# Performance work log

Hardware: AMD Instinct MI355X
Metric: run time of the kernel (lower is better)

## Reference

```python
import jax, jax.numpy as jnp
import numpy as np

ROUTINGS = 3
NUM_CAPSULES = 16


def squash(s, eps=1e-8):
    # s: [..., dim_capsule]
    norm = jnp.linalg.norm(s, axis=-1, keepdims=True)
    return (norm ** 2) / (1.0 + norm ** 2) * (s / (norm + eps))


def setup_inputs() -> dict:
    key = jax.random.key(0)
    k1, k2 = jax.random.split(key)
    x = jax.random.normal(k1, (64, 1024, 64), dtype=jnp.float32)      # [B, n_in, input_dim]
    weight = jax.random.normal(k2, (16, 64, 32), dtype=jnp.float32)    # [nc, input_dim, dc]
    return {"x": x, "weight": weight}


def reference(x, weight):
    B, n_in, _ = x.shape
    nc = weight.shape[0]
    # prediction vectors u_hat: [B, nc, n_in, dc]
    u_hat = jnp.einsum('bni,cid->bcnd', x, weight)
    # routing logits, softmax taken over the output-capsule axis (dim=1 in torch)
    b = jnp.zeros((B, nc, n_in, 1), dtype=u_hat.dtype)
    v = None
    for i in range(ROUTINGS):
        c = jax.nn.softmax(b, axis=1)                 # [B, nc, n_in, 1]
        s = jnp.sum(c * u_hat, axis=2)                # [B, nc, dc]
        v = squash(s)                                 # [B, nc, dc]
        if i < ROUTINGS - 1:
            # agreement: <u_hat, v> per input capsule
            b = b + jnp.einsum('bcnd,bcd->bcn', u_hat, v)[..., None]
    return v
```

## Files before the change

### kernel.cpp

```cpp
#include <hip/hip_runtime.h>
#include <math.h>

#define B_SZ 64
#define N_IN 1024
#define IDIM 64
#define NC   16
#define DC   32
#define NQ   4
#define QR   256
#define NTHR 1024
#define XS   68
#define AS   20

#define WS_CNT 0
#define WS_CS  1024
#define WS_SP1 17408
#define WS_SP2 279552

__device__ __forceinline__ void st_agent(float* p, float v) {
    __hip_atomic_store(p, v, __ATOMIC_RELAXED, __HIP_MEMORY_SCOPE_AGENT);
}
__device__ __forceinline__ float ld_agent(const float* p) {
    return __hip_atomic_load(p, __ATOMIC_RELAXED, __HIP_MEMORY_SCOPE_AGENT);
}
__device__ __forceinline__ float rdlane_f(float v, int l) {
    return __int_as_float(__builtin_amdgcn_readlane(__float_as_int(v), l));
}

__global__ __launch_bounds__(1024) void k_reset(int* cnt) {
    __hip_atomic_store(&cnt[threadIdx.x], 0, __ATOMIC_RELAXED, __HIP_MEMORY_SCOPE_AGENT);
}

__global__ __launch_bounds__(NTHR, 1)
void k_fused(const float* __restrict__ x, const float* __restrict__ W,
             float* __restrict__ out, int* __restrict__ cnt,
             float* __restrict__ cs, float* __restrict__ sp1, float* __restrict__ sp2) {
    const int b = blockIdx.x & 63, q = blockIdx.x >> 6;
    const int tid = threadIdx.x, lane = tid & 63, wave = tid >> 6;
    const int row = tid & 255, grp = tid >> 8;
    const int rq = wave & 3;

    __shared__ float __align__(16) xT[QR * XS];
    __shared__ float __align__(16) aSmT[QR * AS];
    __shared__ float __align__(16) pSm[4 * 64 * AS];
    __shared__ float __align__(16) wSm[IDIM * AS];
    __shared__ float redSm[NC * IDIM];
    __shared__ float __align__(16) vSm[NC * 36];

    int* mycnt = &cnt[b * 16];
    auto arrive = [&]() {
        __syncthreads();
        if (tid == 0)
            __hip_atomic_fetch_add(mycnt, 1, __ATOMIC_RELEASE, __HIP_MEMORY_SCOPE_AGENT);
    };
    auto wait_ge = [&](int t) {
        if (tid == 0)
            while (__hip_atomic_load(mycnt, __ATOMIC_ACQUIRE,
                                     __HIP_MEMORY_SCOPE_AGENT) < t)
                __builtin_amdgcn_s_sleep(1);
        __syncthreads();
    };

    const float4* xb4 = reinterpret_cast<const float4*>(x + ((size_t)b * N_IN + q * QR) * IDIM);
#pragma unroll
    for (int m = 0; m < 4; m++) {
        const int f = tid + m * NTHR;
        const float4 v4 = xb4[f];
        const int n = f >> 4, i0 = (f & 15) * 4;
        *reinterpret_cast<float4*>(&xT[n * XS + i0]) = v4;
    }
    __syncthreads();

    {
        float s = 0.f;
#pragma unroll
        for (int t = 0; t < 16; t++) s += xT[(wave * 16 + t) * XS + lane];
        redSm[wave * 64 + lane] = s;
    }
    __syncthreads();
    if (tid < 64) {
        float r = 0.f;
#pragma unroll
        for (int w2 = 0; w2 < 16; w2++) r += redSm[w2 * 64 + tid];
        st_agent(&cs[(b * NQ + q) * 64 + tid], r);
    }
    arrive();
    wait_ge(4);
    if (tid < 64) {
        float r = 0.f;
#pragma unroll
        for (int k = 0; k < NQ; k++) r += ld_agent(&cs[(b * NQ + k) * 64 + tid]);
        redSm[tid] = r;
    }
    __syncthreads();

    auto caps = [&](int mode) {
        if (tid < 512) {
            const int c = tid >> 5, dd = tid & 31;
            const float* Wc = W + c * (IDIM * DC) + dd;
            float s = 0.f;
#pragma unroll 8
            for (int i = 0; i < IDIM; i++) {
                const float rv = (mode == 0) ? redSm[i] : redSm[c * 64 + i];
                s += rv * Wc[i * DC];
            }
            if (mode == 0) s *= 0.0625f;
            float n2 = s * s;
#pragma unroll
            for (int m = 16; m >= 1; m >>= 1) n2 += __shfl_xor(n2, m);
            const float g = (n2 / (1.f + n2)) / (sqrtf(n2) + 1e-8f);
            if (mode == 2) { if (q == 0) out[b * (NC * DC) + c * DC + dd] = g * s; }
            else           vSm[c * 36 + dd] = g * s;
        }
        __syncthreads();
        if (mode == 2) return;
        const int i = tid >> 4, c = tid & 15;
        const float4* Wr = reinterpret_cast<const float4*>(W + (size_t)(c * IDIM + i) * DC);
        const float4* vv = reinterpret_cast<const float4*>(&vSm[c * 36]);
        float acc = 0.f;
#pragma unroll
        for (int dq = 0; dq < 8; dq++) {
            const float4 wq = Wr[dq], vq = vv[dq];
            acc += wq.x * vq.x + wq.y * vq.y + wq.z * vq.z + wq.w * vq.w;
        }
        if (mode == 0) wSm[i * AS + c] = acc;
        else           wSm[i * AS + c] += acc;
        __syncthreads();
    };

    auto route = [&](float* sp) -> float {
        const float4 wr4 = *reinterpret_cast<const float4*>(&wSm[lane * AS + grp * 4]);
        {
            float a0 = 0.f, a1 = 0.f, a2 = 0.f, a3 = 0.f;
#pragma unroll
            for (int iq = 0; iq < 16; iq++) {
                const float4 xv = *reinterpret_cast<const float4*>(&xT[row * XS + iq * 4]);
#pragma unroll
                for (int j = 0; j < 4; j++) {
                    const int i = iq * 4 + j;
                    const float xc = (j == 0) ? xv.x : (j == 1) ? xv.y
                                   : (j == 2) ? xv.z : xv.w;
                    a0 += rdlane_f(wr4.x, i) * xc;
                    a1 += rdlane_f(wr4.y, i) * xc;
                    a2 += rdlane_f(wr4.z, i) * xc;
                    a3 += rdlane_f(wr4.w, i) * xc;
                }
            }
            *reinterpret_cast<float4*>(&aSmT[row * AS + grp * 4]) =
                make_float4(a0, a1, a2, a3);
        }
        __syncthreads();
        float cw0, cw1, cw2, cw3;
        {
            const float4 q0 = *reinterpret_cast<const float4*>(&aSmT[row * AS + 0]);
            const float4 q1 = *reinterpret_cast<const float4*>(&aSmT[row * AS + 4]);
            const float4 q2 = *reinterpret_cast<const float4*>(&aSmT[row * AS + 8]);
            const float4 q3 = *reinterpret_cast<const float4*>(&aSmT[row * AS + 12]);
            float av[NC] = {q0.x, q0.y, q0.z, q0.w, q1.x, q1.y, q1.z, q1.w,
                            q2.x, q2.y, q2.z, q2.w, q3.x, q3.y, q3.z, q3.w};
            float mx = av[0];
#pragma unroll
            for (int k = 1; k < NC; k++) mx = fmaxf(mx, av[k]);
            float ss = 0.f;
#pragma unroll
            for (int k = 0; k < NC; k++) { av[k] = __expf(av[k] - mx); ss += av[k]; }
            const float inv = 1.f / ss;
            if (grp == 0)      { cw0 = av[0];  cw1 = av[1];  cw2 = av[2];  cw3 = av[3];  }
            else if (grp == 1) { cw0 = av[4];  cw1 = av[5];  cw2 = av[6];  cw3 = av[7];  }
            else if (grp == 2) { cw0 = av[8];  cw1 = av[9];  cw2 = av[10]; cw3 = av[11]; }
            else               { cw0 = av[12]; cw1 = av[13]; cw2 = av[14]; cw3 = av[15]; }
            cw0 *= inv; cw1 *= inv; cw2 *= inv; cw3 *= inv;
        }
        {
            float s0 = 0.f, s1 = 0.f, s2 = 0.f, s3 = 0.f;
#pragma unroll
            for (int nl = 0; nl < 64; nl++) {
                const float xv = xT[(rq * 64 + nl) * XS + lane];
                s0 += rdlane_f(cw0, nl) * xv;
                s1 += rdlane_f(cw1, nl) * xv;
                s2 += rdlane_f(cw2, nl) * xv;
                s3 += rdlane_f(cw3, nl) * xv;
            }
            *reinterpret_cast<float4*>(&pSm[(rq * 64 + lane) * AS + grp * 4]) =
                make_float4(s0, s1, s2, s3);
        }
        __syncthreads();
        const float val = pSm[(0 * 64 + lane) * AS + wave] +
                          pSm[(1 * 64 + lane) * AS + wave] +
                          pSm[(2 * 64 + lane) * AS + wave] +
                          pSm[(3 * 64 + lane) * AS + wave];
        st_agent(&sp[(size_t)(b * NQ + q) * 1024 + tid], val);
        return val;
    };

    caps(0);
    const float v1 = route(sp1);
    arrive();
    wait_ge(8);
    {
        float r = v1;
#pragma unroll
        for (int k = 0; k < NQ; k++)
            if (k != q) r += ld_agent(&sp1[(size_t)(b * NQ + k) * 1024 + tid]);
        redSm[tid] = r;
    }
    __syncthreads();
    caps(1);
    const float v2 = route(sp2);
    arrive();
    if (q != 0) return;
    wait_ge(12);
    {
        float r = v2;
#pragma unroll
        for (int k = 0; k < NQ; k++)
            if (k != q) r += ld_agent(&sp2[(size_t)(b * NQ + k) * 1024 + tid]);
        redSm[tid] = r;
    }
    __syncthreads();
    caps(2);
}

extern "C" void kernel_launch(void* const* d_in, const int* in_sizes, int n_in,
                              void* d_out, int out_size, void* d_ws, size_t ws_size,
                              hipStream_t stream) {
    const float* x = (const float*)d_in[0];
    const float* W = (const float*)d_in[1];
    float* out = (float*)d_out;
    float* ws = (float*)d_ws;

    int*   cnt = (int*)(ws + WS_CNT);
    float* cs  = ws + WS_CS;
    float* sp1 = ws + WS_SP1;
    float* sp2 = ws + WS_SP2;

    k_reset<<<1, 1024, 0, stream>>>(cnt);
    k_fused<<<B_SZ * NQ, NTHR, 0, stream>>>(x, W, out, cnt, cs, sp1, sp2);
}
```

Measured before the change: 49.92 us.

## Split persistent fused kernel into multi-launch pipeline with finer chunking

Replaces the single fused kernel, which used per-batch atomic counters and spin-waits across 4 blocks per batch, with six separate launches: column sums, capsule/squash steps, and routing passes. Each launch works on 64-row chunks (16 chunks per batch) using 256-thread blocks, so far more, smaller blocks are in flight. Cross-block reductions now go through global memory between launches instead of inter-block barriers. In exchange, x is re-read from global memory in every routing pass and there is per-launch overhead for six kernels.

```diff
diff --git a/kernel.cpp b/kernel.cpp
--- a/kernel.cpp
+++ b/kernel.cpp
@@ -6,219 +6,182 @@
 #define IDIM 64
 #define NC   16
 #define DC   32
-#define NQ   4
-#define QR   256
-#define NTHR 1024
-#define XS   68
-#define AS   20
-
-#define WS_CNT 0
-#define WS_CS  1024
-#define WS_SP1 17408
-#define WS_SP2 279552
-
-__device__ __forceinline__ void st_agent(float* p, float v) {
-    __hip_atomic_store(p, v, __ATOMIC_RELAXED, __HIP_MEMORY_SCOPE_AGENT);
-}
-__device__ __forceinline__ float ld_agent(const float* p) {
-    return __hip_atomic_load(p, __ATOMIC_RELAXED, __HIP_MEMORY_SCOPE_AGENT);
-}
+#define NCH  16
+#define XSS  68
+#define ASS  20
+
+#define WS_CSP 0
+#define WS_SP1 65536
+#define WS_SP2 1114112
+#define WS_WV0 2162688
+#define WS_WVE 2228224
+
 __device__ __forceinline__ float rdlane_f(float v, int l) {
     return __int_as_float(__builtin_amdgcn_readlane(__float_as_int(v), l));
 }
 
-__global__ __launch_bounds__(1024) void k_reset(int* cnt) {
-    __hip_atomic_store(&cnt[threadIdx.x], 0, __ATOMIC_RELAXED, __HIP_MEMORY_SCOPE_AGENT);
-}
-
-__global__ __launch_bounds__(NTHR, 1)
-void k_fused(const float* __restrict__ x, const float* __restrict__ W,
-             float* __restrict__ out, int* __restrict__ cnt,
-             float* __restrict__ cs, float* __restrict__ sp1, float* __restrict__ sp2) {
-    const int b = blockIdx.x & 63, q = blockIdx.x >> 6;
-    const int tid = threadIdx.x, lane = tid & 63, wave = tid >> 6;
-    const int row = tid & 255, grp = tid >> 8;
-    const int rq = wave & 3;
-
-    __shared__ float __align__(16) xT[QR * XS];
-    __shared__ float __align__(16) aSmT[QR * AS];
-    __shared__ float __align__(16) pSm[4 * 64 * AS];
-    __shared__ float __align__(16) wSm[IDIM * AS];
+__global__ __launch_bounds__(256) void k_colsum(const float* __restrict__ x,
+                                                float* __restrict__ csp) {
+    const int b = blockIdx.y, ch = blockIdx.x;
+    const int i = threadIdx.x & 63, p = threadIdx.x >> 6;
+    const float* xb = x + ((size_t)b * N_IN + ch * 64) * IDIM;
+    float s = 0.f;
+#pragma unroll
+    for (int t = 0; t < 16; t++) s += xb[(p * 16 + t) * IDIM + i];
+    __shared__ float red[4][64];
+    red[p][i] = s;
+    __syncthreads();
+    if (p == 0)
+        csp[(b * NCH + ch) * 64 + i] = red[0][i] + red[1][i] + red[2][i] + red[3][i];
+}
+
+template<int MODE>
+__global__ __launch_bounds__(512) void k_caps(const float* __restrict__ partIn,
+                                              const float* __restrict__ W,
+                                              const float* __restrict__ wvPrev,
+                                              float* __restrict__ outp) {
+    const int b = blockIdx.x, tid = threadIdx.x;
     __shared__ float redSm[NC * IDIM];
     __shared__ float __align__(16) vSm[NC * 36];
 
-    int* mycnt = &cnt[b * 16];
-    auto arrive = [&]() {
-        __syncthreads();
-        if (tid == 0)
-            __hip_atomic_fetch_add(mycnt, 1, __ATOMIC_RELEASE, __HIP_MEMORY_SCOPE_AGENT);
-    };
-    auto wait_ge = [&](int t) {
-        if (tid == 0)
-            while (__hip_atomic_load(mycnt, __ATOMIC_ACQUIRE,
-                                     __HIP_MEMORY_SCOPE_AGENT) < t)
-                __builtin_amdgcn_s_sleep(1);
-        __syncthreads();
-    };
-
-    const float4* xb4 = reinterpret_cast<const float4*>(x + ((size_t)b * N_IN + q * QR) * IDIM);
-#pragma unroll
-    for (int m = 0; m < 4; m++) {
-        const int f = tid + m * NTHR;
-        const float4 v4 = xb4[f];
-        const int n = f >> 4, i0 = (f & 15) * 4;
-        *reinterpret_cast<float4*>(&xT[n * XS + i0]) = v4;
-    }
-    __syncthreads();
-
-    {
-        float s = 0.f;
-#pragma unroll
-        for (int t = 0; t < 16; t++) s += xT[(wave * 16 + t) * XS + lane];
-        redSm[wave * 64 + lane] = s;
-    }
-    __syncthreads();
-    if (tid < 64) {
-        float r = 0.f;
-#pragma unroll
-        for (int w2 = 0; w2 < 16; w2++) r += redSm[w2 * 64 + tid];
-        st_agent(&cs[(b * NQ + q) * 64 + tid], r);
-    }
-    arrive();
-    wait_ge(4);
-    if (tid < 64) {
-        float r = 0.f;
-#pragma unroll
-        for (int k = 0; k < NQ; k++) r += ld_agent(&cs[(b * NQ + k) * 64 + tid]);
-        redSm[tid] = r;
-    }
-    __syncthreads();
-
-    auto caps = [&](int mode) {
-        if (tid < 512) {
-            const int c = tid >> 5, dd = tid & 31;
-            const float* Wc = W + c * (IDIM * DC) + dd;
-            float s = 0.f;
+    if (MODE == 0) {
+        if (tid < 64) {
+            float r = 0.f;
+#pragma unroll
+            for (int k = 0; k < NCH; k++) r += partIn[(b * NCH + k) * 64 + tid];
+            redSm[tid] = r;
+        }
+    } else {
+#pragma unroll
+        for (int m = 0; m < 2; m++) {
+            const int o = tid + m * 512;
+            float r = 0.f;
+#pragma unroll
+            for (int k = 0; k < NCH; k++)
+                r += partIn[(size_t)(b * NCH + k) * 1024 + o];
+            redSm[o] = r;
+        }
+    }
+    __syncthreads();
+
+    const int c = tid >> 5, dd = tid & 31;
+    const float* Wc = W + c * (IDIM * DC) + dd;
+    float s = 0.f;
 #pragma unroll 8
-            for (int i = 0; i < IDIM; i++) {
-                const float rv = (mode == 0) ? redSm[i] : redSm[c * 64 + i];
-                s += rv * Wc[i * DC];
-            }
-            if (mode == 0) s *= 0.0625f;
-            float n2 = s * s;
-#pragma unroll
-            for (int m = 16; m >= 1; m >>= 1) n2 += __shfl_xor(n2, m);
-            const float g = (n2 / (1.f + n2)) / (sqrtf(n2) + 1e-8f);
-            if (mode == 2) { if (q == 0) out[b * (NC * DC) + c * DC + dd] = g * s; }
-            else           vSm[c * 36 + dd] = g * s;
-        }
-        __syncthreads();
-        if (mode == 2) return;
-        const int i = tid >> 4, c = tid & 15;
-        const float4* Wr = reinterpret_cast<const float4*>(W + (size_t)(c * IDIM + i) * DC);
-        const float4* vv = reinterpret_cast<const float4*>(&vSm[c * 36]);
+    for (int i = 0; i < IDIM; i++) {
+        const float rv = (MODE == 0) ? redSm[i] : redSm[c * 64 + i];
+        s += rv * Wc[i * DC];
+    }
+    if (MODE == 0) s *= 0.0625f;
+    float n2 = s * s;
+#pragma unroll
+    for (int m = 16; m >= 1; m >>= 1) n2 += __shfl_xor(n2, m);
+    const float g = (n2 / (1.f + n2)) / (sqrtf(n2) + 1e-8f);
+    if (MODE == 2) {
+        outp[b * (NC * DC) + c * DC + dd] = g * s;
+        return;
+    }
+    vSm[c * 36 + dd] = g * s;
+    __syncthreads();
+
+    const int c2 = tid & 15, ib = tid >> 4;
+#pragma unroll
+    for (int h = 0; h < 2; h++) {
+        const int i = ib + 32 * h;
+        const float4* Wr = reinterpret_cast<const float4*>(W + (size_t)(c2 * IDIM + i) * DC);
+        const float4* vv = reinterpret_cast<const float4*>(&vSm[c2 * 36]);
         float acc = 0.f;
 #pragma unroll
         for (int dq = 0; dq < 8; dq++) {
             const float4 wq = Wr[dq], vq = vv[dq];
             acc += wq.x * vq.x + wq.y * vq.y + wq.z * vq.z + wq.w * vq.w;
         }
-        if (mode == 0) wSm[i * AS + c] = acc;
-        else           wSm[i * AS + c] += acc;
-        __syncthreads();
-    };
-
-    auto route = [&](float* sp) -> float {
-        const float4 wr4 = *reinterpret_cast<const float4*>(&wSm[lane * AS + grp * 4]);
-        {
-            float a0 = 0.f, a1 = 0.f, a2 = 0.f, a3 = 0.f;
-#pragma unroll
-            for (int iq = 0; iq < 16; iq++) {
-                const float4 xv = *reinterpret_cast<const float4*>(&xT[row * XS + iq * 4]);
-#pragma unroll
-                for (int j = 0; j < 4; j++) {
-                    const int i = iq * 4 + j;
-                    const float xc = (j == 0) ? xv.x : (j == 1) ? xv.y
-                                   : (j == 2) ? xv.z : xv.w;
-                    a0 += rdlane_f(wr4.x, i) * xc;
-                    a1 += rdlane_f(wr4.y, i) * xc;
-                    a2 += rdlane_f(wr4.z, i) * xc;
-                    a3 += rdlane_f(wr4.w, i) * xc;
-                }
+        const int oi = i * NC + c2;
+        outp[b * 1024 + oi] = acc + ((MODE == 1) ? wvPrev[b * 1024 + oi] : 0.f);
+    }
+}
+
+__global__ __launch_bounds__(256) void k_route(const float* __restrict__ x,
+                                               const float* __restrict__ wvp,
+                                               float* __restrict__ sp) {
+    const int b = blockIdx.y, ch = blockIdx.x;
+    const int tid = threadIdx.x, lane = tid & 63, grp = tid >> 6;
+
+    __shared__ float __align__(16) xT[64 * XSS];
+    __shared__ float __align__(16) aSmT[64 * ASS];
+
+    const float4 wr4 = *reinterpret_cast<const float4*>(
+        &wvp[(size_t)b * 1024 + lane * NC + grp * 4]);
+
+    const float4* xb4 = reinterpret_cast<const float4*>(x + ((size_t)b * N_IN + ch * 64) * IDIM);
+#pragma unroll
+    for (int m = 0; m < 4; m++) {
+        const int f = tid + m * 256;
+        const float4 v4 = xb4[f];
+        const int n = f >> 4, i0 = (f & 15) * 4;
+        *reinterpret_cast<float4*>(&xT[n * XSS + i0]) = v4;
+    }
+    __syncthreads();
+
+    {
+        float a0 = 0.f, a1 = 0.f, a2 = 0.f, a3 = 0.f;
+#pragma unroll
+        for (int iq = 0; iq < 16; iq++) {
+            const float4 xv = *reinterpret_cast<const float4*>(&xT[lane * XSS + iq * 4]);
+#pragma unroll
+            for (int j = 0; j < 4; j++) {
+                const int i = iq * 4 + j;
+                const float xc = (j == 0) ? xv.x : (j == 1) ? xv.y
+                               : (j == 2) ? xv.z : xv.w;
+                a0 += rdlane_f(wr4.x, i) * xc;
+                a1 += rdlane_f(wr4.y, i) * xc;
+                a2 += rdlane_f(wr4.z, i) * xc;
+                a3 += rdlane_f(wr4.w, i) * xc;
             }
-            *reinterpret_cast<float4*>(&aSmT[row * AS + grp * 4]) =
-                make_float4(a0, a1, a2, a3);
-        }
-        __syncthreads();
-        float cw0, cw1, cw2, cw3;
-        {
-            const float4 q0 = *reinterpret_cast<const float4*>(&aSmT[row * AS + 0]);
-            const float4 q1 = *reinterpret_cast<const float4*>(&aSmT[row * AS + 4]);
-            const float4 q2 = *reinterpret_cast<const float4*>(&aSmT[row * AS + 8]);
-            const float4 q3 = *reinterpret_cast<const float4*>(&aSmT[row * AS + 12]);
-            float av[NC] = {q0.x, q0.y, q0.z, q0.w, q1.x, q1.y, q1.z, q1.w,
-                            q2.x, q2.y, q2.z, q2.w, q3.x, q3.y, q3.z, q3.w};
-            float mx = av[0];
-#pragma unroll
-            for (int k = 1; k < NC; k++) mx = fmaxf(mx, av[k]);
-            float ss = 0.f;
-#pragma unroll
-            for (int k = 0; k < NC; k++) { av[k] = __expf(av[k] - mx); ss += av[k]; }
-            const float inv = 1.f / ss;
-            if (grp == 0)      { cw0 = av[0];  cw1 = av[1];  cw2 = av[2];  cw3 = av[3];  }
-            else if (grp == 1) { cw0 = av[4];  cw1 = av[5];  cw2 = av[6];  cw3 = av[7];  }
-            else if (grp == 2) { cw0 = av[8];  cw1 = av[9];  cw2 = av[10]; cw3 = av[11]; }
-            else               { cw0 = av[12]; cw1 = av[13]; cw2 = av[14]; cw3 = av[15]; }
-            cw0 *= inv; cw1 *= inv; cw2 *= inv; cw3 *= inv;
-        }
-        {
-            float s0 = 0.f, s1 = 0.f, s2 = 0.f, s3 = 0.f;
-#pragma unroll
-            for (int nl = 0; nl < 64; nl++) {
-                const float xv = xT[(rq * 64 + nl) * XS + lane];
-                s0 += rdlane_f(cw0, nl) * xv;
-                s1 += rdlane_f(cw1, nl) * xv;
-                s2 += rdlane_f(cw2, nl) * xv;
-                s3 += rdlane_f(cw3, nl) * xv;
-            }
-            *reinterpret_cast<float4*>(&pSm[(rq * 64 + lane) * AS + grp * 4]) =
-                make_float4(s0, s1, s2, s3);
-        }
-        __syncthreads();
-        const float val = pSm[(0 * 64 + lane) * AS + wave] +
-                          pSm[(1 * 64 + lane) * AS + wave] +
-                          pSm[(2 * 64 + lane) * AS + wave] +
-                          pSm[(3 * 64 + lane) * AS + wave];
-        st_agent(&sp[(size_t)(b * NQ + q) * 1024 + tid], val);
-        return val;
-    };
-
-    caps(0);
-    const float v1 = route(sp1);
-    arrive();
-    wait_ge(8);
+        }
+        *reinterpret_cast<float4*>(&aSmT[lane * ASS + grp * 4]) =
+            make_float4(a0, a1, a2, a3);
+    }
+    __syncthreads();
+
+    float cw0, cw1, cw2, cw3;
     {
-        float r = v1;
-#pragma unroll
-        for (int k = 0; k < NQ; k++)
-            if (k != q) r += ld_agent(&sp1[(size_t)(b * NQ + k) * 1024 + tid]);
-        redSm[tid] = r;
-    }
-    __syncthreads();
-    caps(1);
-    const float v2 = route(sp2);
-    arrive();
-    if (q != 0) return;
-    wait_ge(12);
+        const float4 q0 = *reinterpret_cast<const float4*>(&aSmT[lane * ASS + 0]);
+        const float4 q1 = *reinterpret_cast<const float4*>(&aSmT[lane * ASS + 4]);
+        const float4 q2 = *reinterpret_cast<const float4*>(&aSmT[lane * ASS + 8]);
+        const float4 q3 = *reinterpret_cast<const float4*>(&aSmT[lane * ASS + 12]);
+        float av[NC] = {q0.x, q0.y, q0.z, q0.w, q1.x, q1.y, q1.z, q1.w,
+                        q2.x, q2.y, q2.z, q2.w, q3.x, q3.y, q3.z, q3.w};
+        float mx = av[0];
+#pragma unroll
+        for (int k = 1; k < NC; k++) mx = fmaxf(mx, av[k]);
+        float ss = 0.f;
+#pragma unroll
+        for (int k = 0; k < NC; k++) { av[k] = __expf(av[k] - mx); ss += av[k]; }
+        const float inv = 1.f / ss;
+        if (grp == 0)      { cw0 = av[0];  cw1 = av[1];  cw2 = av[2];  cw3 = av[3];  }
+        else if (grp == 1) { cw0 = av[4];  cw1 = av[5];  cw2 = av[6];  cw3 = av[7];  }
+        else if (grp == 2) { cw0 = av[8];  cw1 = av[9];  cw2 = av[10]; cw3 = av[11]; }
+        else               { cw0 = av[12]; cw1 = av[13]; cw2 = av[14]; cw3 = av[15]; }
+        cw0 *= inv; cw1 *= inv; cw2 *= inv; cw3 *= inv;
+    }
+
     {
-        float r = v2;
-#pragma unroll
-        for (int k = 0; k < NQ; k++)
-            if (k != q) r += ld_agent(&sp2[(size_t)(b * NQ + k) * 1024 + tid]);
-        redSm[tid] = r;
-    }
-    __syncthreads();
-    caps(2);
+        float s0 = 0.f, s1 = 0.f, s2 = 0.f, s3 = 0.f;
+#pragma unroll
+        for (int nl = 0; nl < 64; nl++) {
+            const float xv = xT[nl * XSS + lane];
+            s0 += rdlane_f(cw0, nl) * xv;
+            s1 += rdlane_f(cw1, nl) * xv;
+            s2 += rdlane_f(cw2, nl) * xv;
+            s3 += rdlane_f(cw3, nl) * xv;
+        }
+        float* spq = sp + (size_t)(b * NCH + ch) * 1024;
+        spq[(grp * 4 + 0) * 64 + lane] = s0;
+        spq[(grp * 4 + 1) * 64 + lane] = s1;
+        spq[(grp * 4 + 2) * 64 + lane] = s2;
+        spq[(grp * 4 + 3) * 64 + lane] = s3;
+    }
 }
 
 extern "C" void kernel_launch(void* const* d_in, const int* in_sizes, int n_in,
@@ -229,11 +192,16 @@
     float* out = (float*)d_out;
     float* ws = (float*)d_ws;
 
-    int*   cnt = (int*)(ws + WS_CNT);
-    float* cs  = ws + WS_CS;
+    float* csp = ws + WS_CSP;
     float* sp1 = ws + WS_SP1;
     float* sp2 = ws + WS_SP2;
-
-    k_reset<<<1, 1024, 0, stream>>>(cnt);
-    k_fused<<<B_SZ * NQ, NTHR, 0, stream>>>(x, W, out, cnt, cs, sp1, sp2);
-}
+    float* wv0 = ws + WS_WV0;
+    float* wvE = ws + WS_WVE;
+
+    k_colsum<<<dim3(NCH, B_SZ), 256, 0, stream>>>(x, csp);
+    k_caps<0><<<B_SZ, 512, 0, stream>>>(csp, W, wv0, wv0);
+    k_route<<<dim3(NCH, B_SZ), 256, 0, stream>>>(x, wv0, sp1);
+    k_caps<1><<<B_SZ, 512, 0, stream>>>(sp1, W, wv0, wvE);
+    k_route<<<dim3(NCH, B_SZ), 256, 0, stream>>>(x, wvE, sp2);
+    k_caps<2><<<B_SZ, 512, 0, stream>>>(sp2, W, wvE, out);
+}
```

New measurement: 49.80 us. No clear change (-0.3%).

## Split fused routing kernel at second barrier into two launches

Applied to the files above, without the earlier changes.

Replaces the middle inter-block spin-wait with a kernel boundary. Phase 1 computes the first routing pass and writes partial sums, and phase 2 re-stages x, reduces the partials, and finishes. The aim is to avoid the cross-block atomic spin barrier between routing iterations. In exchange it pays an extra launch, re-loads x into LDS, and stores and reloads the initial W·v term through the workspace.

```diff
diff --git a/kernel.cpp b/kernel.cpp
--- a/kernel.cpp
+++ b/kernel.cpp
@@ -16,6 +16,7 @@
 #define WS_CS  1024
 #define WS_SP1 17408
 #define WS_SP2 279552
+#define WS_WV0 541696
 
 __device__ __forceinline__ void st_agent(float* p, float v) {
     __hip_atomic_store(p, v, __ATOMIC_RELAXED, __HIP_MEMORY_SCOPE_AGENT);
@@ -31,14 +32,127 @@
     __hip_atomic_store(&cnt[threadIdx.x], 0, __ATOMIC_RELAXED, __HIP_MEMORY_SCOPE_AGENT);
 }
 
+
+__device__ __forceinline__ void stage_x(const float* __restrict__ x, float* xT,
+                                        int b, int q, int tid) {
+    const float4* xb4 = reinterpret_cast<const float4*>(x + ((size_t)b * N_IN + q * QR) * IDIM);
+#pragma unroll
+    for (int m = 0; m < 4; m++) {
+        const int f = tid + m * NTHR;
+        const float4 v4 = xb4[f];
+        const int n = f >> 4, i0 = (f & 15) * 4;
+        *reinterpret_cast<float4*>(&xT[n * XS + i0]) = v4;
+    }
+}
+
+__device__ __forceinline__ float route_pass(const float* xT, const float* wSm,
+                                            float* aSmT, float* pSm,
+                                            int tid, int lane, int wave,
+                                            int row, int grp, int rq) {
+    const float4 wr4 = *reinterpret_cast<const float4*>(&wSm[lane * AS + grp * 4]);
+    {
+        float a0 = 0.f, a1 = 0.f, a2 = 0.f, a3 = 0.f;
+#pragma unroll
+        for (int iq = 0; iq < 16; iq++) {
+            const float4 xv = *reinterpret_cast<const float4*>(&xT[row * XS + iq * 4]);
+#pragma unroll
+            for (int j = 0; j < 4; j++) {
+                const int i = iq * 4 + j;
+                const float xc = (j == 0) ? xv.x : (j == 1) ? xv.y
+                               : (j == 2) ? xv.z : xv.w;
+                a0 += rdlane_f(wr4.x, i) * xc;
+                a1 += rdlane_f(wr4.y, i) * xc;
+                a2 += rdlane_f(wr4.z, i) * xc;
+                a3 += rdlane_f(wr4.w, i) * xc;
+            }
+        }
+        *reinterpret_cast<float4*>(&aSmT[row * AS + grp * 4]) =
+            make_float4(a0, a1, a2, a3);
+    }
+    __syncthreads();
+    float cw0, cw1, cw2, cw3;
+    {
+        const float4 q0 = *reinterpret_cast<const float4*>(&aSmT[row * AS + 0]);
+        const float4 q1 = *reinterpret_cast<const float4*>(&aSmT[row * AS + 4]);
+        const float4 q2 = *reinterpret_cast<const float4*>(&aSmT[row * AS + 8]);
+        const float4 q3 = *reinterpret_cast<const float4*>(&aSmT[row * AS + 12]);
+        float av[NC] = {q0.x, q0.y, q0.z, q0.w, q1.x, q1.y, q1.z, q1.w,
+                        q2.x, q2.y, q2.z, q2.w, q3.x, q3.y, q3.z, q3.w};
+        float mx = av[0];
+#pragma unroll
+        for (int k = 1; k < NC; k++) mx = fmaxf(mx, av[k]);
+        float ss = 0.f;
+#pragma unroll
+        for (int k = 0; k < NC; k++) { av[k] = __expf(av[k] - mx); ss += av[k]; }
+        const float inv = 1.f / ss;
+        if (grp == 0)      { cw0 = av[0];  cw1 = av[1];  cw2 = av[2];  cw3 = av[3];  }
+        else if (grp == 1) { cw0 = av[4];  cw1 = av[5];  cw2 = av[6];  cw3 = av[7];  }
+        else if (grp == 2) { cw0 = av[8];  cw1 = av[9];  cw2 = av[10]; cw3 = av[11]; }
+        else               { cw0 = av[12]; cw1 = av[13]; cw2 = av[14]; cw3 = av[15]; }
+        cw0 *= inv; cw1 *= inv; cw2 *= inv; cw3 *= inv;
+    }
+    {
+        float s0 = 0.f, s1 = 0.f, s2 = 0.f, s3 = 0.f;
+#pragma unroll
+        for (int nl = 0; nl < 64; nl++) {
+            const float xv = xT[(rq * 64 + nl) * XS + lane];
+            s0 += rdlane_f(cw0, nl) * xv;
+            s1 += rdlane_f(cw1, nl) * xv;
+            s2 += rdlane_f(cw2, nl) * xv;
+            s3 += rdlane_f(cw3, nl) * xv;
+        }
+        *reinterpret_cast<float4*>(&pSm[(rq * 64 + lane) * AS + grp * 4]) =
+            make_float4(s0, s1, s2, s3);
+    }
+    __syncthreads();
+    return pSm[(0 * 64 + lane) * AS + wave] + pSm[(1 * 64 + lane) * AS + wave] +
+           pSm[(2 * 64 + lane) * AS + wave] + pSm[(3 * 64 + lane) * AS + wave];
+}
+
+__device__ __forceinline__ void caps_sv(const float* __restrict__ W, const float* redSm,
+                                        float* vSm, int tid, bool modeRed0, bool toOut,
+                                        float* __restrict__ outp, int b, int q) {
+    if (tid < 512) {
+        const int c = tid >> 5, dd = tid & 31;
+        const float* Wc = W + c * (IDIM * DC) + dd;
+        float s = 0.f;
+#pragma unroll 8
+        for (int i = 0; i < IDIM; i++) {
+            const float rv = modeRed0 ? redSm[i] : redSm[c * 64 + i];
+            s += rv * Wc[i * DC];
+        }
+        if (modeRed0) s *= 0.0625f;
+        float n2 = s * s;
+#pragma unroll
+        for (int m = 16; m >= 1; m >>= 1) n2 += __shfl_xor(n2, m);
+        const float g = (n2 / (1.f + n2)) / (sqrtf(n2) + 1e-8f);
+        if (toOut) { if (q == 0) outp[b * (NC * DC) + c * DC + dd] = g * s; }
+        else       vSm[c * 36 + dd] = g * s;
+    }
+    __syncthreads();
+}
+
+__device__ __forceinline__ float caps_wv(const float* __restrict__ W, const float* vSm,
+                                         int tid) {
+    const int i = tid >> 4, c = tid & 15;
+    const float4* Wr = reinterpret_cast<const float4*>(W + (size_t)(c * IDIM + i) * DC);
+    const float4* vv = reinterpret_cast<const float4*>(&vSm[c * 36]);
+    float acc = 0.f;
+#pragma unroll
+    for (int dq = 0; dq < 8; dq++) {
+        const float4 wq = Wr[dq], vq = vv[dq];
+        acc += wq.x * vq.x + wq.y * vq.y + wq.z * vq.z + wq.w * vq.w;
+    }
+    return acc;
+}
+
 __global__ __launch_bounds__(NTHR, 1)
-void k_fused(const float* __restrict__ x, const float* __restrict__ W,
-             float* __restrict__ out, int* __restrict__ cnt,
-             float* __restrict__ cs, float* __restrict__ sp1, float* __restrict__ sp2) {
+void k_phase1(const float* __restrict__ x, const float* __restrict__ W,
+              int* __restrict__ cnt, float* __restrict__ cs,
+              float* __restrict__ sp1, float* __restrict__ wv0) {
     const int b = blockIdx.x & 63, q = blockIdx.x >> 6;
     const int tid = threadIdx.x, lane = tid & 63, wave = tid >> 6;
-    const int row = tid & 255, grp = tid >> 8;
-    const int rq = wave & 3;
+    const int row = tid & 255, grp = tid >> 8, rq = wave & 3;
 
     __shared__ float __align__(16) xT[QR * XS];
     __shared__ float __align__(16) aSmT[QR * AS];
@@ -47,28 +161,7 @@
     __shared__ float redSm[NC * IDIM];
     __shared__ float __align__(16) vSm[NC * 36];
 
-    int* mycnt = &cnt[b * 16];
-    auto arrive = [&]() {
-        __syncthreads();
-        if (tid == 0)
-            __hip_atomic_fetch_add(mycnt, 1, __ATOMIC_RELEASE, __HIP_MEMORY_SCOPE_AGENT);
-    };
-    auto wait_ge = [&](int t) {
-        if (tid == 0)
-            while (__hip_atomic_load(mycnt, __ATOMIC_ACQUIRE,
-                                     __HIP_MEMORY_SCOPE_AGENT) < t)
-                __builtin_amdgcn_s_sleep(1);
-        __syncthreads();
-    };
-
-    const float4* xb4 = reinterpret_cast<const float4*>(x + ((size_t)b * N_IN + q * QR) * IDIM);
-#pragma unroll
-    for (int m = 0; m < 4; m++) {
-        const int f = tid + m * NTHR;
-        const float4 v4 = xb4[f];
-        const int n = f >> 4, i0 = (f & 15) * 4;
-        *reinterpret_cast<float4*>(&xT[n * XS + i0]) = v4;
-    }
+    stage_x(x, xT, b, q, tid);
     __syncthreads();
 
     {
@@ -84,8 +177,14 @@
         for (int w2 = 0; w2 < 16; w2++) r += redSm[w2 * 64 + tid];
         st_agent(&cs[(b * NQ + q) * 64 + tid], r);
     }
-    arrive();
-    wait_ge(4);
+    __syncthreads();
+    if (tid == 0)
+        __hip_atomic_fetch_add(&cnt[b * 16], 1, __ATOMIC_RELEASE, __HIP_MEMORY_SCOPE_AGENT);
+    if (tid == 0)
+        while (__hip_atomic_load(&cnt[b * 16], __ATOMIC_ACQUIRE,
+                                 __HIP_MEMORY_SCOPE_AGENT) < NQ)
+            __builtin_amdgcn_s_sleep(1);
+    __syncthreads();
     if (tid < 64) {
         float r = 0.f;
 #pragma unroll
@@ -94,131 +193,67 @@
     }
     __syncthreads();
 
-    auto caps = [&](int mode) {
-        if (tid < 512) {
-            const int c = tid >> 5, dd = tid & 31;
-            const float* Wc = W + c * (IDIM * DC) + dd;
-            float s = 0.f;
-#pragma unroll 8
-            for (int i = 0; i < IDIM; i++) {
-                const float rv = (mode == 0) ? redSm[i] : redSm[c * 64 + i];
-                s += rv * Wc[i * DC];
-            }
-            if (mode == 0) s *= 0.0625f;
-            float n2 = s * s;
-#pragma unroll
-            for (int m = 16; m >= 1; m >>= 1) n2 += __shfl_xor(n2, m);
-            const float g = (n2 / (1.f + n2)) / (sqrtf(n2) + 1e-8f);
-            if (mode == 2) { if (q == 0) out[b * (NC * DC) + c * DC + dd] = g * s; }
-            else           vSm[c * 36 + dd] = g * s;
-        }
-        __syncthreads();
-        if (mode == 2) return;
-        const int i = tid >> 4, c = tid & 15;
-        const float4* Wr = reinterpret_cast<const float4*>(W + (size_t)(c * IDIM + i) * DC);
-        const float4* vv = reinterpret_cast<const float4*>(&vSm[c * 36]);
-        float acc = 0.f;
-#pragma unroll
-        for (int dq = 0; dq < 8; dq++) {
-            const float4 wq = Wr[dq], vq = vv[dq];
-            acc += wq.x * vq.x + wq.y * vq.y + wq.z * vq.z + wq.w * vq.w;
-        }
-        if (mode == 0) wSm[i * AS + c] = acc;
-        else           wSm[i * AS + c] += acc;
-        __syncthreads();
-    };
-
-    auto route = [&](float* sp) -> float {
-        const float4 wr4 = *reinterpret_cast<const float4*>(&wSm[lane * AS + grp * 4]);
-        {
-            float a0 = 0.f, a1 = 0.f, a2 = 0.f, a3 = 0.f;
-#pragma unroll
-            for (int iq = 0; iq < 16; iq++) {
-                const float4 xv = *reinterpret_cast<const float4*>(&xT[row * XS + iq * 4]);
-#pragma unroll
-                for (int j = 0; j < 4; j++) {
-                    const int i = iq * 4 + j;
-                    const float xc = (j == 0) ? xv.x : (j == 1) ? xv.y
-                                   : (j == 2) ? xv.z : xv.w;
-                    a0 += rdlane_f(wr4.x, i) * xc;
-                    a1 += rdlane_f(wr4.y, i) * xc;
-                    a2 += rdlane_f(wr4.z, i) * xc;
-                    a3 += rdlane_f(wr4.w, i) * xc;
-                }
-            }
-            *reinterpret_cast<float4*>(&aSmT[row * AS + grp * 4]) =
-                make_float4(a0, a1, a2, a3);
-        }
-        __syncthreads();
-        float cw0, cw1, cw2, cw3;
-        {
-            const float4 q0 = *reinterpret_cast<const float4*>(&aSmT[row * AS + 0]);
-            const float4 q1 = *reinterpret_cast<const float4*>(&aSmT[row * AS + 4]);
-            const float4 q2 = *reinterpret_cast<const float4*>(&aSmT[row * AS + 8]);
-            const float4 q3 = *reinterpret_cast<const float4*>(&aSmT[row * AS + 12]);
-            float av[NC] = {q0.x, q0.y, q0.z, q0.w, q1.x, q1.y, q1.z, q1.w,
-                            q2.x, q2.y, q2.z, q2.w, q3.x, q3.y, q3.z, q3.w};
-            float mx = av[0];
-#pragma unroll
-            for (int k = 1; k < NC; k++) mx = fmaxf(mx, av[k]);
-            float ss = 0.f;
-#pragma unroll
-            for (int k = 0; k < NC; k++) { av[k] = __expf(av[k] - mx); ss += av[k]; }
-            const float inv = 1.f / ss;
-            if (grp == 0)      { cw0 = av[0];  cw1 = av[1];  cw2 = av[2];  cw3 = av[3];  }
-            else if (grp == 1) { cw0 = av[4];  cw1 = av[5];  cw2 = av[6];  cw3 = av[7];  }
-            else if (grp == 2) { cw0 = av[8];  cw1 = av[9];  cw2 = av[10]; cw3 = av[11]; }
-            else               { cw0 = av[12]; cw1 = av[13]; cw2 = av[14]; cw3 = av[15]; }
-            cw0 *= inv; cw1 *= inv; cw2 *= inv; cw3 *= inv;
-        }
-        {
-            float s0 = 0.f, s1 = 0.f, s2 = 0.f, s3 = 0.f;
-#pragma unroll
-            for (int nl = 0; nl < 64; nl++) {
-                const float xv = xT[(rq * 64 + nl) * XS + lane];
-                s0 += rdlane_f(cw0, nl) * xv;
-                s1 += rdlane_f(cw1, nl) * xv;
-                s2 += rdlane_f(cw2, nl) * xv;
-                s3 += rdlane_f(cw3, nl) * xv;
-            }
-            *reinterpret_cast<float4*>(&pSm[(rq * 64 + lane) * AS + grp * 4]) =
-                make_float4(s0, s1, s2, s3);
-        }
-        __syncthreads();
-        const float val = pSm[(0 * 64 + lane) * AS + wave] +
-                          pSm[(1 * 64 + lane) * AS + wave] +
-                          pSm[(2 * 64 + lane) * AS + wave] +
-                          pSm[(3 * 64 + lane) * AS + wave];
-        st_agent(&sp[(size_t)(b * NQ + q) * 1024 + tid], val);
-        return val;
-    };
-
-    caps(0);
-    const float v1 = route(sp1);
-    arrive();
-    wait_ge(8);
-    {
-        float r = v1;
-#pragma unroll
-        for (int k = 0; k < NQ; k++)
-            if (k != q) r += ld_agent(&sp1[(size_t)(b * NQ + k) * 1024 + tid]);
+    caps_sv(W, redSm, vSm, tid, true, false, nullptr, b, q);
+    {
+        const float acc = caps_wv(W, vSm, tid);
+        wSm[(tid >> 4) * AS + (tid & 15)] = acc;
+        if (q == 0) wv0[b * 1024 + tid] = acc;
+    }
+    __syncthreads();
+
+    const float val = route_pass(xT, wSm, aSmT, pSm, tid, lane, wave, row, grp, rq);
+    sp1[(size_t)(b * NQ + q) * 1024 + tid] = val;
+}
+
+__global__ __launch_bounds__(NTHR, 1)
+void k_phase2(const float* __restrict__ x, const float* __restrict__ W,
+              float* __restrict__ out, int* __restrict__ cnt,
+              const float* __restrict__ sp1, float* __restrict__ sp2,
+              const float* __restrict__ wv0) {
+    const int b = blockIdx.x & 63, q = blockIdx.x >> 6;
+    const int tid = threadIdx.x, lane = tid & 63, wave = tid >> 6;
+    const int row = tid & 255, grp = tid >> 8, rq = wave & 3;
+
+    __shared__ float __align__(16) xT[QR * XS];
+    __shared__ float __align__(16) aSmT[QR * AS];
+    __shared__ float __align__(16) pSm[4 * 64 * AS];
+    __shared__ float __align__(16) wSm[IDIM * AS];
+    __shared__ float redSm[NC * IDIM];
+    __shared__ float __align__(16) vSm[NC * 36];
+
+    stage_x(x, xT, b, q, tid);
+    {
+        float r = 0.f;
+#pragma unroll
+        for (int k = 0; k < NQ; k++) r += sp1[(size_t)(b * NQ + k) * 1024 + tid];
         redSm[tid] = r;
     }
     __syncthreads();
-    caps(1);
-    const float v2 = route(sp2);
-    arrive();
+
+    caps_sv(W, redSm, vSm, tid, false, false, nullptr, b, q);
+    wSm[(tid >> 4) * AS + (tid & 15)] = caps_wv(W, vSm, tid) + wv0[b * 1024 + tid];
+    __syncthreads();
+
+    const float val = route_pass(xT, wSm, aSmT, pSm, tid, lane, wave, row, grp, rq);
+    st_agent(&sp2[(size_t)(b * NQ + q) * 1024 + tid], val);
+
+    __syncthreads();
+    if (tid == 0)
+        __hip_atomic_fetch_add(&cnt[b * 16], 1, __ATOMIC_RELEASE, __HIP_MEMORY_SCOPE_AGENT);
     if (q != 0) return;
-    wait_ge(12);
-    {
-        float r = v2;
-#pragma unroll
-        for (int k = 0; k < NQ; k++)
-            if (k != q) r += ld_agent(&sp2[(size_t)(b * NQ + k) * 1024 + tid]);
+    if (tid == 0)
+        while (__hip_atomic_load(&cnt[b * 16], __ATOMIC_ACQUIRE,
+                                 __HIP_MEMORY_SCOPE_AGENT) < 2 * NQ)
+            __builtin_amdgcn_s_sleep(1);
+    __syncthreads();
+    {
+        float r = val;
+#pragma unroll
+        for (int k = 1; k < NQ; k++) r += ld_agent(&sp2[(size_t)(b * NQ + k) * 1024 + tid]);
         redSm[tid] = r;
     }
     __syncthreads();
-    caps(2);
+    caps_sv(W, redSm, vSm, tid, false, true, out, b, q);
 }
 
 extern "C" void kernel_launch(void* const* d_in, const int* in_sizes, int n_in,
@@ -233,7 +268,9 @@
     float* cs  = ws + WS_CS;
     float* sp1 = ws + WS_SP1;
     float* sp2 = ws + WS_SP2;
+    float* wv0 = ws + WS_WV0;
 
     k_reset<<<1, 1024, 0, stream>>>(cnt);
-    k_fused<<<B_SZ * NQ, NTHR, 0, stream>>>(x, W, out, cnt, cs, sp1, sp2);
-}
+    k_phase1<<<B_SZ * NQ, NTHR, 0, stream>>>(x, W, cnt, cs, sp1, wv0);
+    k_phase2<<<B_SZ * NQ, NTHR, 0, stream>>>(x, W, out, cnt, sp1, sp2, wv0);
+}
```

Result: faster. 48.10 us (-3.6%).
